# Kernel tuning notes

Measured on AMD Instinct MI355X. Metric: run time of the kernel, lower is better.

## Reference

```python
import jax, jax.numpy as jnp
import numpy as np

N_NODES = 100000
N_EDGES = 3200000
IN_CH = 512
OUT_CH = 64


def setup_inputs() -> dict:
    key = jax.random.key(0)
    k1, k2, k3 = jax.random.split(key, 3)
    edge_index = jax.random.randint(k1, (2, N_EDGES), 0, N_NODES, dtype=jnp.int64)
    x = jax.random.normal(k2, (N_NODES, IN_CH), dtype=jnp.float32)
    W = jax.random.normal(k3, (IN_CH, OUT_CH), dtype=jnp.float32)
    return {"edge_index": edge_index, "x": x, "W": W}


def _propagate(h, row, col, norm, self_norm):
    # one hop of normalized adjacency: (D^-1/2 (A+I) D^-1/2) @ h
    msg = jax.ops.segment_sum(norm[:, None] * h[col], row, num_segments=h.shape[0])
    return msg + self_norm[:, None] * h


def reference(edge_index, x, W):
    n = x.shape[0]
    row, col = edge_index[0], edge_index[1]
    # remove_self_loops then add_self_loops: mask out i==i edges, add identity
    loop_mask = (row != col).astype(x.dtype)
    deg = jax.ops.segment_sum(loop_mask, row, num_segments=n) + 1.0  # +1 self-loop
    dinv = jax.lax.rsqrt(deg)  # deg >= 1, never inf
    norm = dinv[row] * dinv[col] * loop_mask
    self_norm = dinv * dinv
    # A_hat^2 @ (x W) == A_hat @ (A_hat @ (x W)); avoids sparse-sparse matmul
    h = x @ W
    h = _propagate(h, row, col, norm, self_norm)
    h = _propagate(h, row, col, norm, self_norm)
    return h
```

## Files before the change

kernel.cpp:

```cpp
#include <hip/hip_runtime.h>
#include <hip/hip_bf16.h>


#define OUTC 64
#define INC 512
#define ELLW 72
#define RPB 128
#define NBUCK 782
#define PBLK 512
#define CAP 32

typedef short bf16x8 __attribute__((ext_vector_type(8)));
typedef float f32x4 __attribute__((ext_vector_type(4)));

static __device__ inline short f2bf(float f) {
    union { __hip_bfloat16 b; short s; } u;
    u.b = __float2bfloat16(f);
    return u.s;
}
static __device__ inline float bf2f(unsigned short s) {
    union { float f; unsigned u; } v;
    v.u = ((unsigned)s) << 16;
    return v.f;
}

__global__ __launch_bounds__(256) void bucket_scatter(const int* __restrict__ erow,
                                                      int* __restrict__ cnt_pb,
                                                      unsigned int* __restrict__ buf,
                                                      int nE, int n) {
    __shared__ int lcnt[NBUCK];
    for (int i = threadIdx.x; i < NBUCK; i += 256) lcnt[i] = 0;
    __syncthreads();
    const int blk = blockIdx.x;
    const int chunk = (nE + PBLK - 1) / PBLK;
    const int e0 = blk * chunk;
    const int e1 = min(e0 + chunk, nE);
    for (int e = e0 + 2 * (int)threadIdx.x; e < e1; e += 512) {
        int2 r2 = *(const int2*)(erow + e);
        int2 c2 = *(const int2*)(erow + nE + e);
        int rr[2] = {r2.x, r2.y};
        int cc[2] = {c2.x, c2.y};
#pragma unroll
        for (int k = 0; k < 2; ++k) {
            if (e + k >= e1) break;
            int r = rr[k], c = cc[k];
            if (r == c) continue;
            int b = r >> 7;
            int lr = r & (RPB - 1);
            int p = atomicAdd(&lcnt[b], 1);
            if (p < CAP)
                buf[((size_t)b * PBLK + blk) * CAP + p] =
                    ((unsigned int)lr << 17) | (unsigned int)c;
        }
    }
    __syncthreads();
    for (int i = threadIdx.x; i < NBUCK; i += 256) {
        int v = lcnt[i];
        cnt_pb[(size_t)i * PBLK + blk] = v < CAP ? v : CAP;
    }
}

__global__ __launch_bounds__(256) void ell_from_buckets(const unsigned int* __restrict__ buf,
                                                        const int* __restrict__ cnt_pb,
                                                        int* __restrict__ cnt,
                                                        float* __restrict__ dinv,
                                                        int* __restrict__ ell, int n) {
    __shared__ int segc[PBLK];
    __shared__ int rcnt[RPB];
    __shared__ int slab[RPB * ELLW];
    const int b = blockIdx.x;
    for (int i = threadIdx.x; i < PBLK; i += 256) segc[i] = cnt_pb[(size_t)b * PBLK + i];
    for (int i = threadIdx.x; i < RPB; i += 256) rcnt[i] = 0;
    __syncthreads();
    const unsigned int* bb = buf + (size_t)b * PBLK * CAP;
    const int TOT = PBLK * CAP;
    for (int j = threadIdx.x; j < TOT; j += 256) {
        int s = j >> 5;
        int off = j & (CAP - 1);
        if (off < segc[s]) {
            unsigned int u = bb[j];
            int lr = (int)(u >> 17);
            int c = (int)(u & 0x1FFFFu);
            int p = atomicAdd(&rcnt[lr], 1);
            if (p < ELLW) slab[lr * ELLW + p] = c;
        }
    }
    __syncthreads();
    for (int lr = threadIdx.x; lr < RPB; lr += 256) {
        int r = b * RPB + lr;
        if (r < n) {
            int d = rcnt[lr];
            cnt[r] = d;
            dinv[r] = rsqrtf((float)d + 1.0f);
        }
    }
    int* dst = ell + (size_t)b * RPB * ELLW;
    for (int i = threadIdx.x; i < RPB * ELLW; i += 256) dst[i] = slab[i];
}

__global__ __launch_bounds__(256) void prep_w(const float* __restrict__ W,
                                              short* __restrict__ Whp,
                                              short* __restrict__ Wlp) {
    const int tid = blockIdx.x * 256 + threadIdx.x;
    const int lane = tid & 63;
    const int frag = tid >> 6;
    const int kt = frag >> 2;
    const int nt = frag & 3;
    const int col = nt * 16 + (lane & 15);
    const int kb = kt * 32 + (lane >> 4) * 8;
    short h8[8], l8[8];
#pragma unroll
    for (int j = 0; j < 8; ++j) {
        float w = W[(size_t)(kb + j) * OUTC + col];
        short wh = f2bf(w);
        h8[j] = wh;
        l8[j] = f2bf(w - bf2f((unsigned short)wh));
    }
    size_t o = ((size_t)frag * 64 + lane) * 8;
#pragma unroll
    for (int j = 0; j < 8; ++j) { Whp[o + j] = h8[j]; Wlp[o + j] = l8[j]; }
}

__global__ __launch_bounds__(256) void gemm_mfma(const float* __restrict__ x,
                                                 const short* __restrict__ Whp,
                                                 const short* __restrict__ Wlp,
                                                 const float* __restrict__ dinv,
                                                 unsigned short* __restrict__ h, int n) {
    const int lane = threadIdx.x & 63;
    const int wid = __builtin_amdgcn_readfirstlane(threadIdx.x >> 6);
    const int m0 = (blockIdx.x * 4 + wid) * 16;
    if (m0 >= n) return;
    const int quad = lane >> 4;
    const int row = m0 + (lane & 15);

    f32x4 acc[4];
#pragma unroll
    for (int nt = 0; nt < 4; ++nt) acc[nt] = (f32x4){0.f, 0.f, 0.f, 0.f};

    const float* xrow = x + (size_t)row * INC + quad * 8;

    for (int kt = 0; kt < 16; ++kt) {
        float4 a0 = *(const float4*)(xrow + kt * 32);
        float4 a1 = *(const float4*)(xrow + kt * 32 + 4);
        float av[8] = {a0.x, a0.y, a0.z, a0.w, a1.x, a1.y, a1.z, a1.w};
        bf16x8 ah, al;
#pragma unroll
        for (int j = 0; j < 8; ++j) {
            short hj = f2bf(av[j]);
            ah[j] = hj;
            al[j] = f2bf(av[j] - bf2f((unsigned short)hj));
        }
        const size_t fb = ((size_t)kt * 4 * 64 + lane) * 8;
#pragma unroll
        for (int nt = 0; nt < 4; ++nt) {
            bf16x8 bh = *(const bf16x8*)&Whp[fb + (size_t)nt * 64 * 8];
            bf16x8 bl = *(const bf16x8*)&Wlp[fb + (size_t)nt * 64 * 8];
            acc[nt] = __builtin_amdgcn_mfma_f32_16x16x32_bf16(ah, bh, acc[nt], 0, 0, 0);
            acc[nt] = __builtin_amdgcn_mfma_f32_16x16x32_bf16(ah, bl, acc[nt], 0, 0, 0);
            acc[nt] = __builtin_amdgcn_mfma_f32_16x16x32_bf16(al, bh, acc[nt], 0, 0, 0);
        }
    }
    float dv[4];
#pragma unroll
    for (int reg = 0; reg < 4; ++reg) dv[reg] = dinv[m0 + quad * 4 + reg];
#pragma unroll
    for (int nt = 0; nt < 4; ++nt) {
#pragma unroll
        for (int reg = 0; reg < 4; ++reg) {
            int crow = m0 + quad * 4 + reg;
            h[(size_t)crow * OUTC + nt * 16 + (lane & 15)] =
                (unsigned short)f2bf(dv[reg] * acc[nt][reg]);
        }
    }
}

__global__ __launch_bounds__(256) void prop_ell(const unsigned short* __restrict__ hs,
                                                void* __restrict__ hout,
                                                const int* __restrict__ cnt,
                                                const int* __restrict__ ell,
                                                const float* __restrict__ dinv,
                                                int n, int finalhop) {
    const int lane = threadIdx.x & 63;
    const int wid = __builtin_amdgcn_readfirstlane(threadIdx.x >> 6);
    const int node = blockIdx.x * 4 + wid;
    if (node >= n) return;
    float acc = bf2f(hs[(size_t)node * OUTC + lane]);
    int deg = cnt[node];
    if (deg > ELLW) deg = ELLW;
    const int* rowp = ell + (size_t)node * ELLW;
    int j = 0;
    for (; j + 8 <= deg; j += 8) {
        int4 ca = *(const int4*)(rowp + j);
        int4 cb = *(const int4*)(rowp + j + 4);
        acc += bf2f(hs[(size_t)ca.x * OUTC + lane]);
        acc += bf2f(hs[(size_t)ca.y * OUTC + lane]);
        acc += bf2f(hs[(size_t)ca.z * OUTC + lane]);
        acc += bf2f(hs[(size_t)ca.w * OUTC + lane]);
        acc += bf2f(hs[(size_t)cb.x * OUTC + lane]);
        acc += bf2f(hs[(size_t)cb.y * OUTC + lane]);
        acc += bf2f(hs[(size_t)cb.z * OUTC + lane]);
        acc += bf2f(hs[(size_t)cb.w * OUTC + lane]);
    }
    for (; j < deg; ++j) {
        int cc = rowp[j];
        acc += bf2f(hs[(size_t)cc * OUTC + lane]);
    }
    float di = dinv[node];
    if (finalhop) {
        ((float*)hout)[(size_t)node * OUTC + lane] = di * acc;
    } else {
        ((unsigned short*)hout)[(size_t)node * OUTC + lane] =
            (unsigned short)f2bf(di * di * acc);
    }
}

extern "C" void kernel_launch(void* const* d_in, const int* in_sizes, int n_in,
                              void* d_out, int out_size, void* d_ws, size_t ws_size,
                              hipStream_t stream) {
    const int n = out_size / OUTC;
    const int nE = in_sizes[0] / 2;
    const int* erow = (const int*)d_in[0];
    const float* x = (const float*)d_in[1];
    const float* W = (const float*)d_in[2];
    float* out = (float*)d_out;

    char* base = (char*)d_ws;
    size_t off = 0;
    auto take = [&](size_t nbytes) -> void* {
        void* p = base + off;
        off += (nbytes + 255) & ~(size_t)255;
        return p;
    };
    int* cnt = (int*)take((size_t)n * 4);
    float* dinv = (float*)take((size_t)n * 4);
    int* ell = (int*)take((size_t)NBUCK * RPB * ELLW * 4);
    short* Whp = (short*)take((size_t)INC * OUTC * 2);
    short* Wlp = (short*)take((size_t)INC * OUTC * 2);
    unsigned short* h0 = (unsigned short*)take((size_t)n * OUTC * 2);
    unsigned short* h1 = (unsigned short*)take((size_t)n * OUTC * 2);
    unsigned int* buf = (unsigned int*)take((size_t)NBUCK * PBLK * CAP * 4);
    int* cnt_pb = (int*)take((size_t)NBUCK * PBLK * 4);

    bucket_scatter<<<PBLK, 256, 0, stream>>>(erow, cnt_pb, buf, nE, n);

    ell_from_buckets<<<NBUCK, 256, 0, stream>>>(buf, cnt_pb, cnt, dinv, ell, n);

    prep_w<<<16, 256, 0, stream>>>(W, Whp, Wlp);

    const int nwaves = (n + 15) / 16;
    gemm_mfma<<<(nwaves + 3) / 4, 256, 0, stream>>>(x, Whp, Wlp, dinv, h0, n);

    prop_ell<<<(n + 3) / 4, 256, 0, stream>>>(h0, (void*)h1, cnt, ell, dinv, n, 0);
    prop_ell<<<(n + 3) / 4, 256, 0, stream>>>(h1, (void*)out, cnt, ell, dinv, n, 1);
}
```

Measured before the change: 582.4 us.

## Use fewer wider scatter blocks with overflow list and deeper gather unroll

Halves the number of bucket-scatter blocks and uses 1024-thread blocks with 128-bit nontemporal loads of edge indices. Edges that overflow a per-block bucket's fixed capacity now go to a global overflow list, which every ELL-building block scans. The propagation gather loop is unrolled to 16 neighbors with tree-summed partials for more outstanding loads. It adds a memset and a global atomic path, and every ELL block rescans the overflow list.

```diff
diff --git a/kernel.cpp b/kernel.cpp
--- a/kernel.cpp
+++ b/kernel.cpp
@@ -7,11 +7,13 @@
 #define ELLW 72
 #define RPB 128
 #define NBUCK 782
-#define PBLK 512
+#define PBLK 256
 #define CAP 32
+#define OVFCAP 65536
 
 typedef short bf16x8 __attribute__((ext_vector_type(8)));
 typedef float f32x4 __attribute__((ext_vector_type(4)));
+typedef int i32x4 __attribute__((ext_vector_type(4)));
 
 static __device__ inline short f2bf(float f) {
     union { __hip_bfloat16 b; short s; } u;
@@ -24,37 +26,57 @@
     return v.f;
 }
 
-__global__ __launch_bounds__(256) void bucket_scatter(const int* __restrict__ erow,
-                                                      int* __restrict__ cnt_pb,
-                                                      unsigned int* __restrict__ buf,
-                                                      int nE, int n) {
+__global__ __launch_bounds__(1024) void bucket_scatter(const int* __restrict__ erow,
+                                                       int* __restrict__ cnt_pb,
+                                                       unsigned int* __restrict__ buf,
+                                                       unsigned long long* __restrict__ ovf,
+                                                       int* __restrict__ ovf_cnt,
+                                                       int nE, int n) {
     __shared__ int lcnt[NBUCK];
-    for (int i = threadIdx.x; i < NBUCK; i += 256) lcnt[i] = 0;
+    for (int i = threadIdx.x; i < NBUCK; i += 1024) lcnt[i] = 0;
     __syncthreads();
     const int blk = blockIdx.x;
-    const int chunk = (nE + PBLK - 1) / PBLK;
+    const int chunk = nE / PBLK;
     const int e0 = blk * chunk;
-    const int e1 = min(e0 + chunk, nE);
-    for (int e = e0 + 2 * (int)threadIdx.x; e < e1; e += 512) {
-        int2 r2 = *(const int2*)(erow + e);
-        int2 c2 = *(const int2*)(erow + nE + e);
-        int rr[2] = {r2.x, r2.y};
-        int cc[2] = {c2.x, c2.y};
-#pragma unroll
-        for (int k = 0; k < 2; ++k) {
-            if (e + k >= e1) break;
-            int r = rr[k], c = cc[k];
+    const int e1 = (blk == PBLK - 1) ? nE : e0 + chunk;
+    const int q0 = e0 >> 2, q1 = e1 >> 2;
+    const i32x4* rows4 = (const i32x4*)erow;
+    const i32x4* cols4 = (const i32x4*)(erow + nE);
+    for (int q = q0 + (int)threadIdx.x; q < q1; q += 1024) {
+        i32x4 r4 = __builtin_nontemporal_load(&rows4[q]);
+        i32x4 c4 = __builtin_nontemporal_load(&cols4[q]);
+#pragma unroll
+        for (int k = 0; k < 4; ++k) {
+            int r = r4[k], c = c4[k];
             if (r == c) continue;
             int b = r >> 7;
-            int lr = r & (RPB - 1);
             int p = atomicAdd(&lcnt[b], 1);
-            if (p < CAP)
+            if (p < CAP) {
                 buf[((size_t)b * PBLK + blk) * CAP + p] =
-                    ((unsigned int)lr << 17) | (unsigned int)c;
+                    ((unsigned int)(r & (RPB - 1)) << 17) | (unsigned int)c;
+            } else {
+                int qq = atomicAdd(ovf_cnt, 1);
+                if (qq < OVFCAP)
+                    ovf[qq] = ((unsigned long long)(unsigned)r << 32) | (unsigned)c;
+            }
+        }
+    }
+    for (int e = (q1 << 2) + (int)threadIdx.x; e < e1; e += 1024) {
+        int r = erow[e], c = erow[nE + e];
+        if (r == c) continue;
+        int b = r >> 7;
+        int p = atomicAdd(&lcnt[b], 1);
+        if (p < CAP) {
+            buf[((size_t)b * PBLK + blk) * CAP + p] =
+                ((unsigned int)(r & (RPB - 1)) << 17) | (unsigned int)c;
+        } else {
+            int qq = atomicAdd(ovf_cnt, 1);
+            if (qq < OVFCAP)
+                ovf[qq] = ((unsigned long long)(unsigned)r << 32) | (unsigned)c;
         }
     }
     __syncthreads();
-    for (int i = threadIdx.x; i < NBUCK; i += 256) {
+    for (int i = threadIdx.x; i < NBUCK; i += 1024) {
         int v = lcnt[i];
         cnt_pb[(size_t)i * PBLK + blk] = v < CAP ? v : CAP;
     }
@@ -62,6 +84,8 @@
 
 __global__ __launch_bounds__(256) void ell_from_buckets(const unsigned int* __restrict__ buf,
                                                         const int* __restrict__ cnt_pb,
+                                                        const unsigned long long* __restrict__ ovf,
+                                                        const int* __restrict__ ovf_cnt,
                                                         int* __restrict__ cnt,
                                                         float* __restrict__ dinv,
                                                         int* __restrict__ ell, int n) {
@@ -85,6 +109,17 @@
             if (p < ELLW) slab[lr * ELLW + p] = c;
         }
     }
+    int m = *ovf_cnt;
+    if (m > OVFCAP) m = OVFCAP;
+    for (int i = threadIdx.x; i < m; i += 256) {
+        unsigned long long e = ovf[i];
+        int r = (int)(e >> 32);
+        if ((r >> 7) == b) {
+            int lr = r & (RPB - 1);
+            int p = atomicAdd(&rcnt[lr], 1);
+            if (p < ELLW) slab[lr * ELLW + p] = (int)(unsigned)(e & 0xFFFFFFFFu);
+        }
+    }
     __syncthreads();
     for (int lr = threadIdx.x; lr < RPB; lr += 256) {
         int r = b * RPB + lr;
@@ -189,17 +224,37 @@
     if (deg > ELLW) deg = ELLW;
     const int* rowp = ell + (size_t)node * ELLW;
     int j = 0;
-    for (; j + 8 <= deg; j += 8) {
-        int4 ca = *(const int4*)(rowp + j);
-        int4 cb = *(const int4*)(rowp + j + 4);
-        acc += bf2f(hs[(size_t)ca.x * OUTC + lane]);
-        acc += bf2f(hs[(size_t)ca.y * OUTC + lane]);
-        acc += bf2f(hs[(size_t)ca.z * OUTC + lane]);
-        acc += bf2f(hs[(size_t)ca.w * OUTC + lane]);
-        acc += bf2f(hs[(size_t)cb.x * OUTC + lane]);
-        acc += bf2f(hs[(size_t)cb.y * OUTC + lane]);
-        acc += bf2f(hs[(size_t)cb.z * OUTC + lane]);
-        acc += bf2f(hs[(size_t)cb.w * OUTC + lane]);
+    for (; j + 16 <= deg; j += 16) {
+        int4 c0 = *(const int4*)(rowp + j);
+        int4 c1 = *(const int4*)(rowp + j + 4);
+        int4 c2 = *(const int4*)(rowp + j + 8);
+        int4 c3 = *(const int4*)(rowp + j + 12);
+        float t0 = bf2f(hs[(size_t)c0.x * OUTC + lane]);
+        float t1 = bf2f(hs[(size_t)c0.y * OUTC + lane]);
+        float t2 = bf2f(hs[(size_t)c0.z * OUTC + lane]);
+        float t3 = bf2f(hs[(size_t)c0.w * OUTC + lane]);
+        float t4 = bf2f(hs[(size_t)c1.x * OUTC + lane]);
+        float t5 = bf2f(hs[(size_t)c1.y * OUTC + lane]);
+        float t6 = bf2f(hs[(size_t)c1.z * OUTC + lane]);
+        float t7 = bf2f(hs[(size_t)c1.w * OUTC + lane]);
+        float t8 = bf2f(hs[(size_t)c2.x * OUTC + lane]);
+        float t9 = bf2f(hs[(size_t)c2.y * OUTC + lane]);
+        float ta = bf2f(hs[(size_t)c2.z * OUTC + lane]);
+        float tb = bf2f(hs[(size_t)c2.w * OUTC + lane]);
+        float tc = bf2f(hs[(size_t)c3.x * OUTC + lane]);
+        float td = bf2f(hs[(size_t)c3.y * OUTC + lane]);
+        float te = bf2f(hs[(size_t)c3.z * OUTC + lane]);
+        float tf = bf2f(hs[(size_t)c3.w * OUTC + lane]);
+        acc += ((t0 + t1) + (t2 + t3)) + ((t4 + t5) + (t6 + t7));
+        acc += ((t8 + t9) + (ta + tb)) + ((tc + td) + (te + tf));
+    }
+    for (; j + 4 <= deg; j += 4) {
+        int4 c0 = *(const int4*)(rowp + j);
+        float t0 = bf2f(hs[(size_t)c0.x * OUTC + lane]);
+        float t1 = bf2f(hs[(size_t)c0.y * OUTC + lane]);
+        float t2 = bf2f(hs[(size_t)c0.z * OUTC + lane]);
+        float t3 = bf2f(hs[(size_t)c0.w * OUTC + lane]);
+        acc += (t0 + t1) + (t2 + t3);
     }
     for (; j < deg; ++j) {
         int cc = rowp[j];
@@ -240,10 +295,14 @@
     unsigned short* h1 = (unsigned short*)take((size_t)n * OUTC * 2);
     unsigned int* buf = (unsigned int*)take((size_t)NBUCK * PBLK * CAP * 4);
     int* cnt_pb = (int*)take((size_t)NBUCK * PBLK * 4);
-
-    bucket_scatter<<<PBLK, 256, 0, stream>>>(erow, cnt_pb, buf, nE, n);
-
-    ell_from_buckets<<<NBUCK, 256, 0, stream>>>(buf, cnt_pb, cnt, dinv, ell, n);
+    unsigned long long* ovf = (unsigned long long*)take((size_t)OVFCAP * 8);
+    int* ovf_cnt = (int*)take(256);
+
+    (void)hipMemsetAsync(ovf_cnt, 0, 4, stream);
+
+    bucket_scatter<<<PBLK, 1024, 0, stream>>>(erow, cnt_pb, buf, ovf, ovf_cnt, nE, n);
+
+    ell_from_buckets<<<NBUCK, 256, 0, stream>>>(buf, cnt_pb, ovf, ovf_cnt, cnt, dinv, ell, n);
 
     prep_w<<<16, 256, 0, stream>>>(W, Whp, Wlp);
 
```

After: 497.5 us. 1.17x faster.
